# Kernel optimization log

Hardware: AMD Instinct MI355X
Metric: run time of the kernel (lower is better)

Reference implementation:

```python
import jax, jax.numpy as jnp
import numpy as np

MAX_DISP = 4  # 9x9 = 81 displacement window, matching the CUDA correlation kernel


def setup_inputs() -> dict:
    key = jax.random.key(0)
    k1, k2 = jax.random.split(key)
    B, C, H, W = 4, 128, 128, 192
    first = jax.random.normal(k1, (B, C, H, W), dtype=jnp.float32)
    second = jax.random.normal(k2, (B, C, H, W), dtype=jnp.float32)
    return {"first": first, "second": second}


def reference(first, second):
    # first, second: [B, C, H, W]. Output: [B, 81, H, W] cost volume.
    # out[b, (dy+4)*9 + (dx+4), y, x] = mean_c first[b,c,y,x] * second[b,c,y+dy,x+dx]
    # (the CUDA kernel normalizes by the channel count)
    B, C, H, W = first.shape
    p = MAX_DISP
    sec_pad = jnp.pad(second, ((0, 0), (0, 0), (p, p), (p, p)))  # [B, C, H+8, W+8]
    corrs = []
    for dy in range(2 * p + 1):
        for dx in range(2 * p + 1):
            shifted = jax.lax.dynamic_slice(
                sec_pad, (0, 0, dy, dx), (B, C, H, W))
            # channel dot product per pixel -> [B, H, W]
            corrs.append(jnp.einsum('bchw,bchw->bhw', first, shifted))
    out = jnp.stack(corrs, axis=1) / jnp.asarray(C, first.dtype)  # [B, 81, H, W]
    return out
```

## Files before the change

kernel.cpp:

```cpp
#include <hip/hip_runtime.h>


#define B_    4
#define C_    128
#define H_    128
#define W_    192
#define HW_   (H_ * W_)
#define CHW_  (C_ * HW_)

#define TX    64
#define TY    8

__global__ __launch_bounds__(128, 3)
void corr_kernel(const float* __restrict__ first,
                 const float* __restrict__ second,
                 float* __restrict__ out)
{
    const int t  = threadIdx.x;
    const int tx = t & 15;
    const int ty = t >> 4;
    const int x0 = blockIdx.x * TX;
    const int y0 = blockIdx.y * TY;
    const int bz = blockIdx.z;
    const int b  = bz / 9;
    const int dyi = bz - 9 * b;
    const int dy  = dyi - 4;

    const int X = x0 + 4 * tx;
    const int y = y0 + ty;
    const int ys = y + dy;

    const float* fptr = first + (size_t)b * CHW_ + (size_t)y * W_ + X;
    const float* wptr = second + (size_t)b * CHW_ + (size_t)ys * W_ + (X - 4);

    const bool rowv = (ys >= 0) && (ys < H_);
    const bool v0 = rowv && (X >= 4);
    const bool v1 = rowv;
    const bool v2 = rowv && (X <= W_ - 8);

    const float4 z4 = make_float4(0.f, 0.f, 0.f, 0.f);

    float4 A0, A1, A2, AF, B0, B1, B2, BF, C0, C1, C2, CF, D0, D1, D2, DF;

    A0 = v0 ? *(const float4*)(wptr + 0 * HW_)     : z4;
    A1 = v1 ? *(const float4*)(wptr + 0 * HW_ + 4) : z4;
    A2 = v2 ? *(const float4*)(wptr + 0 * HW_ + 8) : z4;
    AF = *(const float4*)(fptr + 0 * HW_);
    B0 = v0 ? *(const float4*)(wptr + 1 * HW_)     : z4;
    B1 = v1 ? *(const float4*)(wptr + 1 * HW_ + 4) : z4;
    B2 = v2 ? *(const float4*)(wptr + 1 * HW_ + 8) : z4;
    BF = *(const float4*)(fptr + 1 * HW_);
    C0 = v0 ? *(const float4*)(wptr + 2 * HW_)     : z4;
    C1 = v1 ? *(const float4*)(wptr + 2 * HW_ + 4) : z4;
    C2 = v2 ? *(const float4*)(wptr + 2 * HW_ + 8) : z4;
    CF = *(const float4*)(fptr + 2 * HW_);
    D0 = v0 ? *(const float4*)(wptr + 3 * HW_)     : z4;
    D1 = v1 ? *(const float4*)(wptr + 3 * HW_ + 4) : z4;
    D2 = v2 ? *(const float4*)(wptr + 3 * HW_ + 8) : z4;
    DF = *(const float4*)(fptr + 3 * HW_);

    float4 acc[9];
    #pragma unroll
    for (int i = 0; i < 9; ++i) acc[i] = z4;

#define STEP(P0, P1, P2, PF, CN)                                        \
    {                                                                   \
        float w[12];                                                    \
        *(float4*)(w + 0) = P0;                                         \
        *(float4*)(w + 4) = P1;                                         \
        *(float4*)(w + 8) = P2;                                         \
        const float4 fc = PF;                                           \
        const size_t co = (size_t)(CN) * HW_;                           \
        P0 = v0 ? *(const float4*)(wptr + co)     : z4;                 \
        P1 = v1 ? *(const float4*)(wptr + co + 4) : z4;                 \
        P2 = v2 ? *(const float4*)(wptr + co + 8) : z4;                 \
        PF = *(const float4*)(fptr + co);                               \
        _Pragma("unroll")                                               \
        for (int dxi = 0; dxi < 9; ++dxi) {                             \
            acc[dxi].x += fc.x * w[dxi + 0];                            \
            acc[dxi].y += fc.y * w[dxi + 1];                            \
            acc[dxi].z += fc.z * w[dxi + 2];                            \
            acc[dxi].w += fc.w * w[dxi + 3];                            \
        }                                                               \
    }

#define STEPL(P0, P1, P2, PF)                                           \
    {                                                                   \
        float w[12];                                                    \
        *(float4*)(w + 0) = P0;                                         \
        *(float4*)(w + 4) = P1;                                         \
        *(float4*)(w + 8) = P2;                                         \
        const float4 fc = PF;                                           \
        _Pragma("unroll")                                               \
        for (int dxi = 0; dxi < 9; ++dxi) {                             \
            acc[dxi].x += fc.x * w[dxi + 0];                            \
            acc[dxi].y += fc.y * w[dxi + 1];                            \
            acc[dxi].z += fc.z * w[dxi + 2];                            \
            acc[dxi].w += fc.w * w[dxi + 3];                            \
        }                                                               \
    }

    #pragma unroll 1
    for (int cb = 0; cb < 124; cb += 4) {
        STEP(A0, A1, A2, AF, cb + 4)
        STEP(B0, B1, B2, BF, cb + 5)
        STEP(C0, C1, C2, CF, cb + 6)
        STEP(D0, D1, D2, DF, cb + 7)
    }
    STEPL(A0, A1, A2, AF)
    STEPL(B0, B1, B2, BF)
    STEPL(C0, C1, C2, CF)
    STEPL(D0, D1, D2, DF)

    const float scale = 1.0f / (float)C_;
    #pragma unroll
    for (int dxi = 0; dxi < 9; ++dxi) {
        const int d = dyi * 9 + dxi;
        float4 r = acc[dxi];
        r.x *= scale; r.y *= scale; r.z *= scale; r.w *= scale;
        *(float4*)(out + ((size_t)b * 81 + d) * HW_ + (size_t)y * W_ + X) = r;
    }
}

extern "C" void kernel_launch(void* const* d_in, const int* in_sizes, int n_in,
                              void* d_out, int out_size, void* d_ws, size_t ws_size,
                              hipStream_t stream) {
    const float* first  = (const float*)d_in[0];
    const float* second = (const float*)d_in[1];
    float* out = (float*)d_out;

    dim3 grid(W_ / TX, H_ / TY, B_ * 9);
    dim3 block(128);
    corr_kernel<<<grid, block, 0, stream>>>(first, second, out);
}
```

Before: 207.7 us.

## Hand-schedule channel loop in inline asm with explicit vmcnt pipelining

Replaces the compiler-generated channel loop with hand-written inline assembly. Loads go into fixed VGPR ranges with global_load_dwordx4, and the FMA blocks are pinned to explicit s_waitcnt vmcnt values so a four-deep load pipeline stays in flight. Out-of-bounds loads are redirected to a zero page with a zero stride instead of being predicated. This removes per-load select logic and compiler scheduling conservatism. In exchange it hardcodes the register allocation, relies on the clobber lists to keep the compiler away from those registers, and the fixed vmcnt values assume no other outstanding memory ops.

```diff
diff --git a/kernel.cpp b/kernel.cpp
--- a/kernel.cpp
+++ b/kernel.cpp
@@ -1,4 +1,5 @@
 #include <hip/hip_runtime.h>
+#include <stdint.h>
 
 
 #define B_    4
@@ -7,9 +8,106 @@
 #define W_    192
 #define HW_   (H_ * W_)
 #define CHW_  (C_ * HW_)
+#define CHB   ((uint64_t)HW_ * 4)
 
 #define TX    64
 #define TY    8
+
+__device__ __align__(16) float ZPAGE[4];
+
+#define PIPE_CLOB \
+    "v32","v33","v34","v35","v36","v37","v38","v39","v40","v41", \
+    "v42","v43","v44","v45","v46","v47","v48","v49","v50","v51", \
+    "v52","v53","v54","v55","v56","v57","v58","v59","v60","v61", \
+    "v62","v63","v64","v65","v66","v67","v68","v69","v70","v71", \
+    "v72","v73","v74","v75","v76","v77","v78","v79","v80","v81", \
+    "v82","v83","v84","v85","v86","v87","v88","v89","v90","v91", \
+    "v92","v93","v94","v95","v96","v97","v98","v99","v100","v101", \
+    "v102","v103","v104","v105","v106","v107","v108","v109","v110","v111", \
+    "v112","v113","v114","v115","v116","v117","v118","v119","v120","v121", \
+    "v122","v123","v124","v125","v126","v127","v128","v129","v130","v131"
+
+#define FM(a,f,w) "v_fmac_f32 v" #a ", v" #f ", v" #w "\n\t"
+#define ZM(n)     "v_mov_b32 v" #n ", 0\n\t"
+
+#define FMA_A asm volatile( \
+    FM(96,44,32)  FM(97,45,33)  FM(98,46,34)  FM(99,47,35)   \
+    FM(100,44,33) FM(101,45,34) FM(102,46,35) FM(103,47,36)  \
+    FM(104,44,34) FM(105,45,35) FM(106,46,36) FM(107,47,37)  \
+    FM(108,44,35) FM(109,45,36) FM(110,46,37) FM(111,47,38)  \
+    FM(112,44,36) FM(113,45,37) FM(114,46,38) FM(115,47,39)  \
+    FM(116,44,37) FM(117,45,38) FM(118,46,39) FM(119,47,40)  \
+    FM(120,44,38) FM(121,45,39) FM(122,46,40) FM(123,47,41)  \
+    FM(124,44,39) FM(125,45,40) FM(126,46,41) FM(127,47,42)  \
+    FM(128,44,40) FM(129,45,41) FM(130,46,42) FM(131,47,43)  \
+    ::: PIPE_CLOB)
+
+#define FMA_B asm volatile( \
+    FM(96,60,48)  FM(97,61,49)  FM(98,62,50)  FM(99,63,51)   \
+    FM(100,60,49) FM(101,61,50) FM(102,62,51) FM(103,63,52)  \
+    FM(104,60,50) FM(105,61,51) FM(106,62,52) FM(107,63,53)  \
+    FM(108,60,51) FM(109,61,52) FM(110,62,53) FM(111,63,54)  \
+    FM(112,60,52) FM(113,61,53) FM(114,62,54) FM(115,63,55)  \
+    FM(116,60,53) FM(117,61,54) FM(118,62,55) FM(119,63,56)  \
+    FM(120,60,54) FM(121,61,55) FM(122,62,56) FM(123,63,57)  \
+    FM(124,60,55) FM(125,61,56) FM(126,62,57) FM(127,63,58)  \
+    FM(128,60,56) FM(129,61,57) FM(130,62,58) FM(131,63,59)  \
+    ::: PIPE_CLOB)
+
+#define FMA_C asm volatile( \
+    FM(96,76,64)  FM(97,77,65)  FM(98,78,66)  FM(99,79,67)   \
+    FM(100,76,65) FM(101,77,66) FM(102,78,67) FM(103,79,68)  \
+    FM(104,76,66) FM(105,77,67) FM(106,78,68) FM(107,79,69)  \
+    FM(108,76,67) FM(109,77,68) FM(110,78,69) FM(111,79,70)  \
+    FM(112,76,68) FM(113,77,69) FM(114,78,70) FM(115,79,71)  \
+    FM(116,76,69) FM(117,77,70) FM(118,78,71) FM(119,79,72)  \
+    FM(120,76,70) FM(121,77,71) FM(122,78,72) FM(123,79,73)  \
+    FM(124,76,71) FM(125,77,72) FM(126,78,73) FM(127,79,74)  \
+    FM(128,76,72) FM(129,77,73) FM(130,78,74) FM(131,79,75)  \
+    ::: PIPE_CLOB)
+
+#define FMA_D asm volatile( \
+    FM(96,92,80)  FM(97,93,81)  FM(98,94,82)  FM(99,95,83)   \
+    FM(100,92,81) FM(101,93,82) FM(102,94,83) FM(103,95,84)  \
+    FM(104,92,82) FM(105,93,83) FM(106,94,84) FM(107,95,85)  \
+    FM(108,92,83) FM(109,93,84) FM(110,94,85) FM(111,95,86)  \
+    FM(112,92,84) FM(113,93,85) FM(114,94,86) FM(115,95,87)  \
+    FM(116,92,85) FM(117,93,86) FM(118,94,87) FM(119,95,88)  \
+    FM(120,92,86) FM(121,93,87) FM(122,94,88) FM(123,95,89)  \
+    FM(124,92,87) FM(125,93,88) FM(126,94,89) FM(127,95,90)  \
+    FM(128,92,88) FM(129,93,89) FM(130,94,90) FM(131,95,91)  \
+    ::: PIPE_CLOB)
+
+#define ISSUE_A asm volatile( \
+    "global_load_dwordx4 v[32:35], %0, off\n\t" \
+    "global_load_dwordx4 v[36:39], %1, off\n\t" \
+    "global_load_dwordx4 v[40:43], %2, off\n\t" \
+    "global_load_dwordx4 v[44:47], %3, off" \
+    :: "v"(q0), "v"(q1), "v"(q2), "v"(qf) : PIPE_CLOB)
+#define ISSUE_B asm volatile( \
+    "global_load_dwordx4 v[48:51], %0, off\n\t" \
+    "global_load_dwordx4 v[52:55], %1, off\n\t" \
+    "global_load_dwordx4 v[56:59], %2, off\n\t" \
+    "global_load_dwordx4 v[60:63], %3, off" \
+    :: "v"(q0), "v"(q1), "v"(q2), "v"(qf) : PIPE_CLOB)
+#define ISSUE_C asm volatile( \
+    "global_load_dwordx4 v[64:67], %0, off\n\t" \
+    "global_load_dwordx4 v[68:71], %1, off\n\t" \
+    "global_load_dwordx4 v[72:75], %2, off\n\t" \
+    "global_load_dwordx4 v[76:79], %3, off" \
+    :: "v"(q0), "v"(q1), "v"(q2), "v"(qf) : PIPE_CLOB)
+#define ISSUE_D asm volatile( \
+    "global_load_dwordx4 v[80:83], %0, off\n\t" \
+    "global_load_dwordx4 v[84:87], %1, off\n\t" \
+    "global_load_dwordx4 v[88:91], %2, off\n\t" \
+    "global_load_dwordx4 v[92:95], %3, off" \
+    :: "v"(q0), "v"(q1), "v"(q2), "v"(qf) : PIPE_CLOB)
+
+#define WAITVM(N) \
+    asm volatile("s_waitcnt vmcnt(" #N ")" ::: "memory"); \
+    __builtin_amdgcn_sched_barrier(0);
+
+#define ADV  { q0 += s0; q1 += s1; q2 += s2; qf += CHB; }
 
 __global__ __launch_bounds__(128, 3)
 void corr_kernel(const float* __restrict__ first,
@@ -30,94 +128,93 @@
     const int y = y0 + ty;
     const int ys = y + dy;
 
-    const float* fptr = first + (size_t)b * CHW_ + (size_t)y * W_ + X;
-    const float* wptr = second + (size_t)b * CHW_ + (size_t)ys * W_ + (X - 4);
+    const float* fptr  = first  + (size_t)b * CHW_ + (size_t)y * W_ + X;
+    const float* wbase = second + (size_t)b * CHW_ + (size_t)ys * W_ + (X - 4);
 
     const bool rowv = (ys >= 0) && (ys < H_);
     const bool v0 = rowv && (X >= 4);
     const bool v1 = rowv;
     const bool v2 = rowv && (X <= W_ - 8);
 
-    const float4 z4 = make_float4(0.f, 0.f, 0.f, 0.f);
-
-    float4 A0, A1, A2, AF, B0, B1, B2, BF, C0, C1, C2, CF, D0, D1, D2, DF;
-
-    A0 = v0 ? *(const float4*)(wptr + 0 * HW_)     : z4;
-    A1 = v1 ? *(const float4*)(wptr + 0 * HW_ + 4) : z4;
-    A2 = v2 ? *(const float4*)(wptr + 0 * HW_ + 8) : z4;
-    AF = *(const float4*)(fptr + 0 * HW_);
-    B0 = v0 ? *(const float4*)(wptr + 1 * HW_)     : z4;
-    B1 = v1 ? *(const float4*)(wptr + 1 * HW_ + 4) : z4;
-    B2 = v2 ? *(const float4*)(wptr + 1 * HW_ + 8) : z4;
-    BF = *(const float4*)(fptr + 1 * HW_);
-    C0 = v0 ? *(const float4*)(wptr + 2 * HW_)     : z4;
-    C1 = v1 ? *(const float4*)(wptr + 2 * HW_ + 4) : z4;
-    C2 = v2 ? *(const float4*)(wptr + 2 * HW_ + 8) : z4;
-    CF = *(const float4*)(fptr + 2 * HW_);
-    D0 = v0 ? *(const float4*)(wptr + 3 * HW_)     : z4;
-    D1 = v1 ? *(const float4*)(wptr + 3 * HW_ + 4) : z4;
-    D2 = v2 ? *(const float4*)(wptr + 3 * HW_ + 8) : z4;
-    DF = *(const float4*)(fptr + 3 * HW_);
-
-    float4 acc[9];
-    #pragma unroll
-    for (int i = 0; i < 9; ++i) acc[i] = z4;
-
-#define STEP(P0, P1, P2, PF, CN)                                        \
-    {                                                                   \
-        float w[12];                                                    \
-        *(float4*)(w + 0) = P0;                                         \
-        *(float4*)(w + 4) = P1;                                         \
-        *(float4*)(w + 8) = P2;                                         \
-        const float4 fc = PF;                                           \
-        const size_t co = (size_t)(CN) * HW_;                           \
-        P0 = v0 ? *(const float4*)(wptr + co)     : z4;                 \
-        P1 = v1 ? *(const float4*)(wptr + co + 4) : z4;                 \
-        P2 = v2 ? *(const float4*)(wptr + co + 8) : z4;                 \
-        PF = *(const float4*)(fptr + co);                               \
-        _Pragma("unroll")                                               \
-        for (int dxi = 0; dxi < 9; ++dxi) {                             \
-            acc[dxi].x += fc.x * w[dxi + 0];                            \
-            acc[dxi].y += fc.y * w[dxi + 1];                            \
-            acc[dxi].z += fc.z * w[dxi + 2];                            \
-            acc[dxi].w += fc.w * w[dxi + 3];                            \
-        }                                                               \
+    const uint64_t zp = (uint64_t)(uintptr_t)ZPAGE;
+    uint64_t q0 = v0 ? (uint64_t)(uintptr_t)(wbase)     : zp;
+    uint64_t q1 = v1 ? (uint64_t)(uintptr_t)(wbase + 4) : zp;
+    uint64_t q2 = v2 ? (uint64_t)(uintptr_t)(wbase + 8) : zp;
+    uint64_t qf = (uint64_t)(uintptr_t)fptr;
+    const uint64_t s0 = v0 ? CHB : 0;
+    const uint64_t s1 = v1 ? CHB : 0;
+    const uint64_t s2 = v2 ? CHB : 0;
+
+    asm volatile(
+        ZM(96)  ZM(97)  ZM(98)  ZM(99)  ZM(100) ZM(101) ZM(102) ZM(103)
+        ZM(104) ZM(105) ZM(106) ZM(107) ZM(108) ZM(109) ZM(110) ZM(111)
+        ZM(112) ZM(113) ZM(114) ZM(115) ZM(116) ZM(117) ZM(118) ZM(119)
+        ZM(120) ZM(121) ZM(122) ZM(123) ZM(124) ZM(125) ZM(126) ZM(127)
+        ZM(128) ZM(129) ZM(130) ZM(131)
+        ::: PIPE_CLOB);
+
+    ISSUE_A; ADV
+    ISSUE_B; ADV
+    ISSUE_C; ADV
+    ISSUE_D; ADV
+
+    #pragma unroll 1
+    for (int it = 0; it < 31; ++it) {
+        WAITVM(12) FMA_A; ISSUE_A; ADV
+        WAITVM(12) FMA_B; ISSUE_B; ADV
+        WAITVM(12) FMA_C; ISSUE_C; ADV
+        WAITVM(12) FMA_D; ISSUE_D; ADV
     }
-
-#define STEPL(P0, P1, P2, PF)                                           \
-    {                                                                   \
-        float w[12];                                                    \
-        *(float4*)(w + 0) = P0;                                         \
-        *(float4*)(w + 4) = P1;                                         \
-        *(float4*)(w + 8) = P2;                                         \
-        const float4 fc = PF;                                           \
-        _Pragma("unroll")                                               \
-        for (int dxi = 0; dxi < 9; ++dxi) {                             \
-            acc[dxi].x += fc.x * w[dxi + 0];                            \
-            acc[dxi].y += fc.y * w[dxi + 1];                            \
-            acc[dxi].z += fc.z * w[dxi + 2];                            \
-            acc[dxi].w += fc.w * w[dxi + 3];                            \
-        }                                                               \
-    }
-
-    #pragma unroll 1
-    for (int cb = 0; cb < 124; cb += 4) {
-        STEP(A0, A1, A2, AF, cb + 4)
-        STEP(B0, B1, B2, BF, cb + 5)
-        STEP(C0, C1, C2, CF, cb + 6)
-        STEP(D0, D1, D2, DF, cb + 7)
-    }
-    STEPL(A0, A1, A2, AF)
-    STEPL(B0, B1, B2, BF)
-    STEPL(C0, C1, C2, CF)
-    STEPL(D0, D1, D2, DF)
+    WAITVM(12) FMA_A;
+    WAITVM(8)  FMA_B;
+    WAITVM(4)  FMA_C;
+    WAITVM(0)  FMA_D;
+
+    float rr[36];
+    asm volatile(
+        "v_mov_b32 %0, v96\n\t"  "v_mov_b32 %1, v97\n\t"
+        "v_mov_b32 %2, v98\n\t"  "v_mov_b32 %3, v99\n\t"
+        "v_mov_b32 %4, v100\n\t" "v_mov_b32 %5, v101\n\t"
+        "v_mov_b32 %6, v102\n\t" "v_mov_b32 %7, v103\n\t"
+        "v_mov_b32 %8, v104\n\t" "v_mov_b32 %9, v105\n\t"
+        "v_mov_b32 %10, v106\n\t" "v_mov_b32 %11, v107\n\t"
+        "v_mov_b32 %12, v108\n\t" "v_mov_b32 %13, v109\n\t"
+        "v_mov_b32 %14, v110\n\t" "v_mov_b32 %15, v111\n\t"
+        "v_mov_b32 %16, v112\n\t" "v_mov_b32 %17, v113"
+        : "=v"(rr[0]), "=v"(rr[1]), "=v"(rr[2]), "=v"(rr[3]),
+          "=v"(rr[4]), "=v"(rr[5]), "=v"(rr[6]), "=v"(rr[7]),
+          "=v"(rr[8]), "=v"(rr[9]), "=v"(rr[10]), "=v"(rr[11]),
+          "=v"(rr[12]), "=v"(rr[13]), "=v"(rr[14]), "=v"(rr[15]),
+          "=v"(rr[16]), "=v"(rr[17])
+        :: "v96","v97","v98","v99","v100","v101","v102","v103","v104",
+           "v105","v106","v107","v108","v109","v110","v111","v112","v113");
+    asm volatile(
+        "v_mov_b32 %0, v114\n\t" "v_mov_b32 %1, v115\n\t"
+        "v_mov_b32 %2, v116\n\t" "v_mov_b32 %3, v117\n\t"
+        "v_mov_b32 %4, v118\n\t" "v_mov_b32 %5, v119\n\t"
+        "v_mov_b32 %6, v120\n\t" "v_mov_b32 %7, v121\n\t"
+        "v_mov_b32 %8, v122\n\t" "v_mov_b32 %9, v123\n\t"
+        "v_mov_b32 %10, v124\n\t" "v_mov_b32 %11, v125\n\t"
+        "v_mov_b32 %12, v126\n\t" "v_mov_b32 %13, v127\n\t"
+        "v_mov_b32 %14, v128\n\t" "v_mov_b32 %15, v129\n\t"
+        "v_mov_b32 %16, v130\n\t" "v_mov_b32 %17, v131"
+        : "=v"(rr[18]), "=v"(rr[19]), "=v"(rr[20]), "=v"(rr[21]),
+          "=v"(rr[22]), "=v"(rr[23]), "=v"(rr[24]), "=v"(rr[25]),
+          "=v"(rr[26]), "=v"(rr[27]), "=v"(rr[28]), "=v"(rr[29]),
+          "=v"(rr[30]), "=v"(rr[31]), "=v"(rr[32]), "=v"(rr[33]),
+          "=v"(rr[34]), "=v"(rr[35])
+        :: "v114","v115","v116","v117","v118","v119","v120","v121","v122",
+           "v123","v124","v125","v126","v127","v128","v129","v130","v131");
 
     const float scale = 1.0f / (float)C_;
     #pragma unroll
     for (int dxi = 0; dxi < 9; ++dxi) {
         const int d = dyi * 9 + dxi;
-        float4 r = acc[dxi];
-        r.x *= scale; r.y *= scale; r.z *= scale; r.w *= scale;
+        float4 r;
+        r.x = rr[4 * dxi + 0] * scale;
+        r.y = rr[4 * dxi + 1] * scale;
+        r.z = rr[4 * dxi + 2] * scale;
+        r.w = rr[4 * dxi + 3] * scale;
         *(float4*)(out + ((size_t)b * 81 + d) * HW_ + (size_t)y * W_ + X) = r;
     }
 }
```

New measurement: 195.9 us. 1.06x faster.
